# Optimization experiments

Measured on AMD Instinct MI355X. Metric: run time of the kernel, lower is better.

Reference implementation:

```python
import jax, jax.numpy as jnp
import numpy as np

N_NODES = 50000
N_EDGES = 800000
IN_F = 128
HID = 128
OUT = 2


def setup_inputs() -> dict:
    key = jax.random.key(0)
    ks = jax.random.split(key, 10)
    x = jax.random.normal(ks[0], (N_NODES, IN_F), dtype=jnp.float32)
    edge_index = jax.random.randint(ks[1], (2, N_EDGES), 0, N_NODES, dtype=jnp.int64)

    def lin(k, fan_in, fan_out):
        s = 1.0 / np.sqrt(fan_in)
        return jax.random.uniform(k, (fan_in, fan_out), jnp.float32, -s, s)

    return {
        "x": x,
        "edge_index": edge_index,
        # SAGEConv1: lin_l applied to mean-aggregated neighbors (with bias),
        # lin_r applied to root features (no bias), PyG convention.
        "W1_l": lin(ks[2], IN_F, HID),
        "W1_r": lin(ks[3], IN_F, HID),
        "b1": jnp.zeros((HID,), jnp.float32),
        "W2_l": lin(ks[4], HID, HID),
        "W2_r": lin(ks[5], HID, HID),
        "b2": jnp.zeros((HID,), jnp.float32),
        "Wfc": lin(ks[6], HID, OUT),
        "bfc": jnp.zeros((OUT,), jnp.float32),
    }


def reference(x, edge_index, W1_l, W1_r, b1, W2_l, W2_r, b2, Wfc, bfc):
    n = x.shape[0]
    src = edge_index[0]  # message source j
    dst = edge_index[1]  # aggregation target i
    # in-degree for mean aggregation (clamp to avoid div-by-zero for isolated nodes)
    deg = jax.ops.segment_sum(jnp.ones_like(dst, dtype=x.dtype), dst, num_segments=n)
    inv_deg = 1.0 / jnp.maximum(deg, 1.0)  # [n]

    def sage_conv(h, Wl, Wr, b):
        # mean over incoming neighbor features, then two linear maps
        agg = jax.ops.segment_sum(h[src], dst, num_segments=n) * inv_deg[:, None]
        return agg @ Wl + h @ Wr + b

    # dropout is identity at inference (training=False)
    h = jax.nn.relu(sage_conv(x, W1_l, W1_r, b1))
    h = jax.nn.relu(sage_conv(h, W2_l, W2_r, b2))
    return h @ Wfc + bfc  # [n, out] logits
```

## Files before the change

kernel.cpp:

```cpp
#include <hip/hip_runtime.h>

#define NN 50000
#define NE 800000
#define BSHIFT 9
#define NB_BUCKET ((NN + 511) >> BSHIFT)
#define BCAP 16384
#define EPB 2048
#define NBLK_E ((NE + EPB - 1) / EPB)

#define CVT_BLKS 6250
#define PREP_BLKS 32
#define SETUP_GRID (CVT_BLKS + PREP_BLKS + 1)

typedef short short8 __attribute__((ext_vector_type(8)));
typedef short short4v __attribute__((ext_vector_type(4)));
typedef float f32x4 __attribute__((ext_vector_type(4)));

__device__ inline unsigned short bf16_rne(float f) {
    unsigned u = __float_as_uint(f);
    unsigned r = (u + 0x7fffu + ((u >> 16) & 1u)) >> 16;
    return (unsigned short)r;
}
__device__ inline float bf16_to_f32(unsigned short h) {
    return __uint_as_float((unsigned)h << 16);
}

__global__ __launch_bounds__(256) void setup_kernel(const float* __restrict__ x,
                                                    unsigned short* __restrict__ xb,
                                                    const float* __restrict__ W0,
                                                    const float* __restrict__ W1,
                                                    const float* __restrict__ W2,
                                                    const float* __restrict__ W3,
                                                    short* __restrict__ wf,
                                                    int* __restrict__ cursor0) {
    int b = blockIdx.x;
    if (b < CVT_BLKS) {
        int i = b * 256 + threadIdx.x;
        float4 v = ((const float4*)x)[i];
        short4v r;
        r[0] = (short)bf16_rne(v.x);
        r[1] = (short)bf16_rne(v.y);
        r[2] = (short)bf16_rne(v.z);
        r[3] = (short)bf16_rne(v.w);
        ((short4v*)xb)[i] = r;
    } else if (b < CVT_BLKS + PREP_BLKS) {
        int t = (b - CVT_BLKS) * 256 + threadIdx.x;
        int mat = t >> 11;
        const float* W = (mat == 0) ? W0 : (mat == 1) ? W1 : (mat == 2) ? W2 : W3;
        short* out = wf + (size_t)mat * 32768;
        int r = t & 2047;
        int nt = r >> 8;
        int kc = (r >> 6) & 3;
        int lane = r & 63;
        int n = nt * 16 + (lane & 15);
        int kbase = kc * 32 + ((lane >> 4) << 3);
        short8 vh, vl;
#pragma unroll
        for (int j = 0; j < 8; ++j) {
            float w = W[(size_t)(kbase + j) * 128 + n];
            unsigned short h = bf16_rne(w);
            unsigned short l = bf16_rne(w - bf16_to_f32(h));
            vh[j] = (short)h;
            vl[j] = (short)l;
        }
        size_t o = ((((size_t)nt * 4 + kc) * 2) * 64 + lane) * 8;
        *(short8*)(out + o) = vh;
        *(short8*)(out + o + 512) = vl;
    } else {
        if (threadIdx.x < NB_BUCKET) cursor0[threadIdx.x] = 0;
    }
}

__global__ __launch_bounds__(256) void binA_kernel(const int* __restrict__ src,
                                                   const int* __restrict__ dst,
                                                   int* __restrict__ cursor0,
                                                   unsigned* __restrict__ packed, int ne) {
    __shared__ int cnt[NB_BUCKET];
    __shared__ int gstart[NB_BUCKET];
    __shared__ int cur[NB_BUCKET];
    int t = threadIdx.x;
    if (t < NB_BUCKET) cnt[t] = 0;
    __syncthreads();
    int base = blockIdx.x * EPB + t * 8;
    int s[8], d[8];
    int m = 0;
    if (base + 8 <= ne) {
        *(int4*)&s[0] = *(const int4*)(src + base);
        *(int4*)&s[4] = *(const int4*)(src + base + 4);
        *(int4*)&d[0] = *(const int4*)(dst + base);
        *(int4*)&d[4] = *(const int4*)(dst + base + 4);
        m = 8;
    } else if (base < ne) {
        m = ne - base;
        for (int i = 0; i < m; ++i) { s[i] = src[base + i]; d[i] = dst[base + i]; }
    }
    for (int i = 0; i < m; ++i) atomicAdd(&cnt[d[i] >> BSHIFT], 1);
    __syncthreads();
    if (t < NB_BUCKET) {
        gstart[t] = t * BCAP + atomicAdd(&cursor0[t], cnt[t]);
        cur[t] = 0;
    }
    __syncthreads();
    for (int i = 0; i < m; ++i) {
        int b = d[i] >> BSHIFT;
        int l = atomicAdd(&cur[b], 1);
        packed[gstart[b] + l] = ((unsigned)(d[i] & 511) << 16) | (unsigned)s[i];
    }
}

__global__ __launch_bounds__(512) void binB_kernel(const unsigned* __restrict__ packed,
                                                   const int* __restrict__ cursor0,
                                                   int* __restrict__ row_ptr,
                                                   float* __restrict__ inv_deg,
                                                   int* __restrict__ col, int n, int ne) {
    __shared__ int sdeg[512];
    __shared__ int scur[512];
    __shared__ int scnt[NB_BUCKET];
    __shared__ int sebeg[NB_BUCKET];
    __shared__ int swv[8];
    int b = blockIdx.x, t = threadIdx.x;
    int lane = t & 63, wid = t >> 6;
    if (t < NB_BUCKET) scnt[t] = cursor0[t];
    sdeg[t] = 0;
    __syncthreads();
    if (t == 0) {
        int run = 0;
        for (int i = 0; i < NB_BUCKET; ++i) { sebeg[i] = run; run += scnt[i]; }
    }
    __syncthreads();
    int ebeg = sebeg[b];
    int cntE = scnt[b];
    const unsigned* pk = packed + (size_t)b * BCAP;
    for (int e = t; e < cntE; e += 512) atomicAdd(&sdeg[pk[e] >> 16], 1);
    __syncthreads();
    int v = sdeg[t];
    int incl = v;
#pragma unroll
    for (int d = 1; d < 64; d <<= 1) {
        int u = __shfl_up(incl, d, 64);
        if (lane >= d) incl += u;
    }
    if (lane == 63) swv[wid] = incl;
    __syncthreads();
    int wbase = 0;
    for (int i = 0; i < 8; ++i) wbase += (i < wid) ? swv[i] : 0;
    int excl = wbase + incl - v;
    scur[t] = excl;
    int node = (b << BSHIFT) + t;
    if (node < n) {
        row_ptr[node] = ebeg + excl;
        inv_deg[node] = 1.0f / (float)(v > 0 ? v : 1);
    }
    if (b == 0 && t == 0) row_ptr[n] = ne;
    __syncthreads();
    for (int e = t; e < cntE; e += 512) {
        unsigned w = pk[e];
        int dl = w >> 16;
        int pos = ebeg + atomicAdd(&scur[dl], 1);
        col[pos] = (int)(w & 0xffffu);
    }
}

__global__ __launch_bounds__(256) void agg_kernel(const unsigned short* __restrict__ hb,
                                                  const int* __restrict__ row_ptr,
                                                  const int* __restrict__ col,
                                                  const float* __restrict__ inv_deg,
                                                  unsigned short* __restrict__ outb, int n) {
    int node = blockIdx.x * 4 + (threadIdx.x >> 6);
    if (node >= n) return;
    int lane = threadIdx.x & 63;
    int slot = lane >> 4, sub = lane & 15;
    int beg = row_ptr[node], end = row_ptr[node + 1];
    const unsigned short* base = hb + (sub << 3);
    float acc[8];
#pragma unroll
    for (int j = 0; j < 8; ++j) acc[j] = 0.f;

    int e = beg + slot;
    for (; e + 4 < end; e += 8) {
        int j0 = col[e];
        int j1 = col[e + 4];
        uint4 v0 = *(const uint4*)(base + ((size_t)j0 << 7));
        uint4 v1 = *(const uint4*)(base + ((size_t)j1 << 7));
        unsigned w0[4] = {v0.x, v0.y, v0.z, v0.w};
        unsigned w1[4] = {v1.x, v1.y, v1.z, v1.w};
#pragma unroll
        for (int d = 0; d < 4; ++d) {
            acc[2 * d + 0] += __uint_as_float(w0[d] << 16);
            acc[2 * d + 1] += __uint_as_float(w0[d] & 0xffff0000u);
            acc[2 * d + 0] += __uint_as_float(w1[d] << 16);
            acc[2 * d + 1] += __uint_as_float(w1[d] & 0xffff0000u);
        }
    }
    if (e < end) {
        int j0 = col[e];
        uint4 v0 = *(const uint4*)(base + ((size_t)j0 << 7));
        unsigned w0[4] = {v0.x, v0.y, v0.z, v0.w};
#pragma unroll
        for (int d = 0; d < 4; ++d) {
            acc[2 * d + 0] += __uint_as_float(w0[d] << 16);
            acc[2 * d + 1] += __uint_as_float(w0[d] & 0xffff0000u);
        }
    }
#pragma unroll
    for (int j = 0; j < 8; ++j) {
        acc[j] += __shfl_xor(acc[j], 16, 64);
        acc[j] += __shfl_xor(acc[j], 32, 64);
    }
    if (slot == 0) {
        float s = inv_deg[node];
        short8 o;
#pragma unroll
        for (int j = 0; j < 8; ++j) o[j] = (short)bf16_rne(acc[j] * s);
        *(short8*)(outb + ((size_t)node << 7) + (sub << 3)) = o;
    }
}

__global__ __launch_bounds__(256) void gemm_mfma(const unsigned short* __restrict__ A0b,
                                                 const unsigned short* __restrict__ A1b,
                                                 const short* __restrict__ Wf0,
                                                 const short* __restrict__ Wf1,
                                                 const float* __restrict__ bias,
                                                 unsigned short* __restrict__ outb,
                                                 const float* __restrict__ Wfc,
                                                 const float* __restrict__ bfc,
                                                 float* __restrict__ fcout,
                                                 int n) {
    int lane = threadIdx.x & 63;
    int wave = threadIdx.x >> 6;
    int quad = lane >> 4, m16 = lane & 15;
    int row_base = blockIdx.x * 64 + wave * 16;
    int arow = row_base + m16;
    if (arow > n - 1) arow = n - 1;

    f32x4 acc[8];
#pragma unroll
    for (int nt = 0; nt < 8; ++nt) acc[nt] = (f32x4){0.f, 0.f, 0.f, 0.f};

    const unsigned short* ap0 = A0b + ((size_t)arow << 7) + (quad << 3);
    const unsigned short* ap1 = A1b + ((size_t)arow << 7) + (quad << 3);
#pragma unroll
    for (int kc = 0; kc < 4; ++kc) {
        short8 a0 = *(const short8*)(ap0 + kc * 32);
        short8 a1 = *(const short8*)(ap1 + kc * 32);
        const short* wp0 = Wf0 + ((size_t)kc * 2 * 64 + lane) * 8;
        const short* wp1 = Wf1 + ((size_t)kc * 2 * 64 + lane) * 8;
#pragma unroll
        for (int nt = 0; nt < 8; ++nt) {
            short8 bh0 = *(const short8*)(wp0 + (size_t)nt * 4096);
            short8 bl0 = *(const short8*)(wp0 + (size_t)nt * 4096 + 512);
            short8 bh1 = *(const short8*)(wp1 + (size_t)nt * 4096);
            short8 bl1 = *(const short8*)(wp1 + (size_t)nt * 4096 + 512);
            acc[nt] = __builtin_amdgcn_mfma_f32_16x16x32_bf16(bh0, a0, acc[nt], 0, 0, 0);
            acc[nt] = __builtin_amdgcn_mfma_f32_16x16x32_bf16(bl0, a0, acc[nt], 0, 0, 0);
            acc[nt] = __builtin_amdgcn_mfma_f32_16x16x32_bf16(bh1, a1, acc[nt], 0, 0, 0);
            acc[nt] = __builtin_amdgcn_mfma_f32_16x16x32_bf16(bl1, a1, acc[nt], 0, 0, 0);
        }
    }

    int onode = row_base + m16;
    if (outb) {
        if (onode < n) {
            unsigned short* op = outb + ((size_t)onode << 7) + (quad << 2);
#pragma unroll
            for (int nt = 0; nt < 8; ++nt) {
                float4 bs = *(const float4*)(bias + nt * 16 + (quad << 2));
                short4v o;
                o[0] = (short)bf16_rne(fmaxf(acc[nt][0] + bs.x, 0.f));
                o[1] = (short)bf16_rne(fmaxf(acc[nt][1] + bs.y, 0.f));
                o[2] = (short)bf16_rne(fmaxf(acc[nt][2] + bs.z, 0.f));
                o[3] = (short)bf16_rne(fmaxf(acc[nt][3] + bs.w, 0.f));
                *(short4v*)(op + nt * 16) = o;
            }
        }
    } else {
        float p0 = 0.f, p1 = 0.f;
#pragma unroll
        for (int nt = 0; nt < 8; ++nt) {
            float4 bs = *(const float4*)(bias + nt * 16 + (quad << 2));
            float bv[4] = {bs.x, bs.y, bs.z, bs.w};
#pragma unroll
            for (int r = 0; r < 4; ++r) {
                float v = fmaxf(acc[nt][r] + bv[r], 0.f);
                int hid = nt * 16 + (quad << 2) + r;
                float2 wv = *(const float2*)(Wfc + 2 * hid);
                p0 += v * wv.x;
                p1 += v * wv.y;
            }
        }
        p0 += __shfl_xor(p0, 16, 64);
        p0 += __shfl_xor(p0, 32, 64);
        p1 += __shfl_xor(p1, 16, 64);
        p1 += __shfl_xor(p1, 32, 64);
        if (quad == 0 && onode < n) {
            float2 o;
            o.x = p0 + bfc[0];
            o.y = p1 + bfc[1];
            *(float2*)(fcout + 2 * (size_t)onode) = o;
        }
    }
}

extern "C" void kernel_launch(void* const* d_in, const int* in_sizes, int n_in,
                              void* d_out, int out_size, void* d_ws, size_t ws_size,
                              hipStream_t stream) {
    const float* x   = (const float*)d_in[0];
    const int* edge  = (const int*)d_in[1];
    const float* W1l = (const float*)d_in[2];
    const float* W1r = (const float*)d_in[3];
    const float* b1  = (const float*)d_in[4];
    const float* W2l = (const float*)d_in[5];
    const float* W2r = (const float*)d_in[6];
    const float* b2  = (const float*)d_in[7];
    const float* Wfc = (const float*)d_in[8];
    const float* bfc = (const float*)d_in[9];
    float* out = (float*)d_out;

    const int n = NN, ne = NE;
    const int* src = edge;
    const int* dst = edge + ne;

    char* ws = (char*)d_ws;
    size_t off = 0;
    auto alloc = [&](size_t bytes) -> char* {
        char* p = ws + off;
        off = (off + bytes + 511) & ~(size_t)511;
        return p;
    };
    int* row_ptr     = (int*)alloc((size_t)(n + 1) * 4);
    float* invdeg    = (float*)alloc((size_t)n * 4);
    int* cursor0     = (int*)alloc((size_t)NB_BUCKET * 4);
    short* wf        = (short*)alloc((size_t)4 * 32768 * 2);
    unsigned* packed = (unsigned*)alloc((size_t)NB_BUCKET * BCAP * 4);
    int* col         = (int*)alloc((size_t)ne * 4);
    unsigned short* aggb = (unsigned short*)alloc((size_t)n * 128 * 2);
    unsigned short* xb   = (unsigned short*)alloc((size_t)n * 128 * 2);
    unsigned short* h1b  = (unsigned short*)alloc((size_t)n * 128 * 2);
    (void)ws_size; (void)in_sizes; (void)n_in; (void)out_size;

    setup_kernel<<<SETUP_GRID, 256, 0, stream>>>(x, xb, W1l, W1r, W2l, W2r, wf, cursor0);
    binA_kernel<<<NBLK_E, 256, 0, stream>>>(src, dst, cursor0, packed, ne);
    binB_kernel<<<NB_BUCKET, 512, 0, stream>>>(packed, cursor0, row_ptr, invdeg, col, n, ne);

    agg_kernel<<<(n + 3) / 4, 256, 0, stream>>>(xb, row_ptr, col, invdeg, aggb, n);
    gemm_mfma<<<(n + 63) / 64, 256, 0, stream>>>(aggb, xb, wf, wf + 32768, b1, h1b,
                                                 (const float*)0, (const float*)0, (float*)0, n);
    agg_kernel<<<(n + 3) / 4, 256, 0, stream>>>(h1b, row_ptr, col, invdeg, aggb, n);
    gemm_mfma<<<(n + 63) / 64, 256, 0, stream>>>(aggb, h1b, wf + 2 * 32768, wf + 3 * 32768, b2,
                                                 (unsigned short*)0, Wfc, bfc, out, n);
}
```

Baseline: 230.1 us.

## Split aggregation feature dim into four column slices with persistent grid

The neighbor-mean aggregation kernel now splits each node's 128-wide bf16 row into four 32-column slices. Consecutive blocks handle different slices of the same node groups, and a fixed grid of 8192 blocks loops persistently over node groups. Each lane gathers one dword per neighbor instead of 16 bytes, with four independent gathers unrolled per iteration to raise memory-level parallelism. The intent is to shrink the per-block working set and improve L2 locality across slice blocks. In exchange, col indices and row_ptr are read four times, and each gather moves less data per request.

```diff
diff --git a/kernel.cpp b/kernel.cpp
--- a/kernel.cpp
+++ b/kernel.cpp
@@ -11,6 +11,8 @@
 #define CVT_BLKS 6250
 #define PREP_BLKS 32
 #define SETUP_GRID (CVT_BLKS + PREP_BLKS + 1)
+
+#define AGG_GRID 8192
 
 typedef short short8 __attribute__((ext_vector_type(8)));
 typedef short short4v __attribute__((ext_vector_type(4)));
@@ -166,53 +168,51 @@
                                                   const int* __restrict__ col,
                                                   const float* __restrict__ inv_deg,
                                                   unsigned short* __restrict__ outb, int n) {
-    int node = blockIdx.x * 4 + (threadIdx.x >> 6);
-    if (node >= n) return;
-    int lane = threadIdx.x & 63;
-    int slot = lane >> 4, sub = lane & 15;
-    int beg = row_ptr[node], end = row_ptr[node + 1];
-    const unsigned short* base = hb + (sub << 3);
-    float acc[8];
-#pragma unroll
-    for (int j = 0; j < 8; ++j) acc[j] = 0.f;
-
-    int e = beg + slot;
-    for (; e + 4 < end; e += 8) {
-        int j0 = col[e];
-        int j1 = col[e + 4];
-        uint4 v0 = *(const uint4*)(base + ((size_t)j0 << 7));
-        uint4 v1 = *(const uint4*)(base + ((size_t)j1 << 7));
-        unsigned w0[4] = {v0.x, v0.y, v0.z, v0.w};
-        unsigned w1[4] = {v1.x, v1.y, v1.z, v1.w};
-#pragma unroll
-        for (int d = 0; d < 4; ++d) {
-            acc[2 * d + 0] += __uint_as_float(w0[d] << 16);
-            acc[2 * d + 1] += __uint_as_float(w0[d] & 0xffff0000u);
-            acc[2 * d + 0] += __uint_as_float(w1[d] << 16);
-            acc[2 * d + 1] += __uint_as_float(w1[d] & 0xffff0000u);
-        }
-    }
-    if (e < end) {
-        int j0 = col[e];
-        uint4 v0 = *(const uint4*)(base + ((size_t)j0 << 7));
-        unsigned w0[4] = {v0.x, v0.y, v0.z, v0.w};
-#pragma unroll
-        for (int d = 0; d < 4; ++d) {
-            acc[2 * d + 0] += __uint_as_float(w0[d] << 16);
-            acc[2 * d + 1] += __uint_as_float(w0[d] & 0xffff0000u);
-        }
-    }
-#pragma unroll
-    for (int j = 0; j < 8; ++j) {
-        acc[j] += __shfl_xor(acc[j], 16, 64);
-        acc[j] += __shfl_xor(acc[j], 32, 64);
-    }
-    if (slot == 0) {
-        float s = inv_deg[node];
-        short8 o;
-#pragma unroll
-        for (int j = 0; j < 8; ++j) o[j] = (short)bf16_rne(acc[j] * s);
-        *(short8*)(outb + ((size_t)node << 7) + (sub << 3)) = o;
+    int slice = blockIdx.x & 3;
+    int wave = threadIdx.x >> 6, lane = threadIdx.x & 63;
+    int eslot = lane >> 4, dw = lane & 15;
+    const unsigned* hd = (const unsigned*)hb + (slice << 4) + dw;
+    int ngrp = (n + 3) >> 2;
+    for (int g = blockIdx.x >> 2; g < ngrp; g += (AGG_GRID >> 2)) {
+        int node = g * 4 + wave;
+        if (node >= n) continue;
+        int beg = row_ptr[node], end = row_ptr[node + 1];
+        float a0 = 0.f, a1 = 0.f;
+        int e = beg + eslot;
+        for (; e + 12 < end; e += 16) {
+            int j0 = col[e];
+            int j1 = col[e + 4];
+            int j2 = col[e + 8];
+            int j3 = col[e + 12];
+            unsigned v0 = hd[(size_t)j0 << 6];
+            unsigned v1 = hd[(size_t)j1 << 6];
+            unsigned v2 = hd[(size_t)j2 << 6];
+            unsigned v3 = hd[(size_t)j3 << 6];
+            a0 += __uint_as_float(v0 << 16);
+            a1 += __uint_as_float(v0 & 0xffff0000u);
+            a0 += __uint_as_float(v1 << 16);
+            a1 += __uint_as_float(v1 & 0xffff0000u);
+            a0 += __uint_as_float(v2 << 16);
+            a1 += __uint_as_float(v2 & 0xffff0000u);
+            a0 += __uint_as_float(v3 << 16);
+            a1 += __uint_as_float(v3 & 0xffff0000u);
+        }
+        for (; e < end; e += 4) {
+            unsigned v0 = hd[(size_t)col[e] << 6];
+            a0 += __uint_as_float(v0 << 16);
+            a1 += __uint_as_float(v0 & 0xffff0000u);
+        }
+        a0 += __shfl_xor(a0, 16, 64);
+        a0 += __shfl_xor(a0, 32, 64);
+        a1 += __shfl_xor(a1, 16, 64);
+        a1 += __shfl_xor(a1, 32, 64);
+        if (eslot == 0) {
+            float s = inv_deg[node];
+            unsigned short h0 = bf16_rne(a0 * s);
+            unsigned short h1 = bf16_rne(a1 * s);
+            ((unsigned*)outb)[((size_t)node << 6) + (slice << 4) + dw] =
+                (unsigned)h0 | ((unsigned)h1 << 16);
+        }
     }
 }
 
@@ -342,10 +342,10 @@
     binA_kernel<<<NBLK_E, 256, 0, stream>>>(src, dst, cursor0, packed, ne);
     binB_kernel<<<NB_BUCKET, 512, 0, stream>>>(packed, cursor0, row_ptr, invdeg, col, n, ne);
 
-    agg_kernel<<<(n + 3) / 4, 256, 0, stream>>>(xb, row_ptr, col, invdeg, aggb, n);
+    agg_kernel<<<AGG_GRID, 256, 0, stream>>>(xb, row_ptr, col, invdeg, aggb, n);
     gemm_mfma<<<(n + 63) / 64, 256, 0, stream>>>(aggb, xb, wf, wf + 32768, b1, h1b,
                                                  (const float*)0, (const float*)0, (float*)0, n);
-    agg_kernel<<<(n + 3) / 4, 256, 0, stream>>>(h1b, row_ptr, col, invdeg, aggb, n);
+    agg_kernel<<<AGG_GRID, 256, 0, stream>>>(h1b, row_ptr, col, invdeg, aggb, n);
     gemm_mfma<<<(n + 63) / 64, 256, 0, stream>>>(aggb, h1b, wf + 2 * 32768, wf + 3 * 32768, b2,
                                                  (unsigned short*)0, Wfc, bfc, out, n);
 }
```

Measured after the change: 317.7 us. +38.1%, slower.
